# Kernel tuning notes

Measured on AMD Instinct MI355X. Metric: run time of the kernel, lower is better.

The kernel has to match this reference:

```python
import jax, jax.numpy as jnp
import numpy as np

HIDDEN = 2048
N_HEADS = 32
N_KV_HEADS = 8
HEAD_DIM = HIDDEN // N_HEADS  # 64
N_REP = N_HEADS // N_KV_HEADS  # 4
ROPE_THETA = 10000.0


def setup_inputs() -> dict:
    key = jax.random.key(0)
    ks = jax.random.split(key, 5)
    b, s = 2, 2048
    x = jax.random.normal(ks[0], (b, s, HIDDEN), dtype=jnp.float32)
    position_ids = jnp.arange(b * s, dtype=jnp.int32).reshape(b, s)
    sc = 1.0 / np.sqrt(HIDDEN)
    Wq = jax.random.normal(ks[1], (HIDDEN, HIDDEN), dtype=jnp.float32) * sc
    Wk = jax.random.normal(ks[2], (HIDDEN, N_KV_HEADS * HEAD_DIM), dtype=jnp.float32) * sc
    Wv = jax.random.normal(ks[3], (HIDDEN, N_KV_HEADS * HEAD_DIM), dtype=jnp.float32) * sc
    Wo = jax.random.normal(ks[4], (HIDDEN, HIDDEN), dtype=jnp.float32) * sc
    return {"input_ids": x, "Wq": Wq, "Wk": Wk, "Wv": Wv, "Wo": Wo,
            "position_ids": position_ids}


def _rope_cos_sin(position_ids, dtype):
    # inv_freq: [head_dim/2]
    inv_freq = 1.0 / (ROPE_THETA ** (jnp.arange(0, HEAD_DIM, 2, dtype=jnp.float32) / HEAD_DIM))
    freqs = position_ids.astype(jnp.float32)[..., None] * inv_freq  # [b, s, d/2]
    emb = jnp.concatenate([freqs, freqs], axis=-1)  # [b, s, d]
    return emb.astype(dtype), None  # placeholder, replaced below


def _rotate_half(x):
    x1, x2 = jnp.split(x, 2, axis=-1)
    return jnp.concatenate([-x2, x1], axis=-1)


def reference(input_ids, Wq, Wk, Wv, Wo, position_ids):
    b, s, _ = input_ids.shape
    q = (input_ids @ Wq).reshape(b, s, N_HEADS, HEAD_DIM).transpose(0, 2, 1, 3)      # [b,H,s,d]
    k = (input_ids @ Wk).reshape(b, s, N_KV_HEADS, HEAD_DIM).transpose(0, 2, 1, 3)   # [b,Hkv,s,d]
    v = (input_ids @ Wv).reshape(b, s, N_KV_HEADS, HEAD_DIM).transpose(0, 2, 1, 3)

    # RoPE
    inv_freq = 1.0 / (ROPE_THETA ** (jnp.arange(0, HEAD_DIM, 2, dtype=jnp.float32) / HEAD_DIM))
    freqs = position_ids.astype(jnp.float32)[..., None] * inv_freq  # [b,s,d/2]
    emb = jnp.concatenate([freqs, freqs], axis=-1)                   # [b,s,d]
    cos = jnp.cos(emb).astype(input_ids.dtype)[:, None, :, :]        # [b,1,s,d]
    sin = jnp.sin(emb).astype(input_ids.dtype)[:, None, :, :]
    q = q * cos + _rotate_half(q) * sin
    k = k * cos + _rotate_half(k) * sin

    # repeat_kv: [b,Hkv,s,d] -> [b,H,s,d]
    k = jnp.repeat(k, N_REP, axis=1)
    v = jnp.repeat(v, N_REP, axis=1)

    # causal SDPA
    scale = 1.0 / np.sqrt(HEAD_DIM)
    scores = jnp.einsum('bhqd,bhkd->bhqk', q, k) * scale
    causal = jnp.tril(jnp.ones((s, s), dtype=bool))
    scores = jnp.where(causal, scores, jnp.finfo(scores.dtype).min)
    attn = jax.nn.softmax(scores, axis=-1)
    out = jnp.einsum('bhqk,bhkd->bhqd', attn, v)                     # [b,H,s,d]
    out = out.transpose(0, 2, 1, 3).reshape(b, s, HIDDEN)
    return out @ Wo
```

## Files before the change

### kernel.cpp

```cpp
#include <hip/hip_runtime.h>
#include <hip/hip_bf16.h>

#define HIDDEN 2048
#define NHEADS 32
#define NKVH   8
#define HD     64
#define BATCH  2
#define SEQ    2048
#define ROWS   (BATCH * SEQ)
#define NQKV   3072
#define KCOL   2048
#define VCOL   2560

typedef __bf16 bf16x8 __attribute__((ext_vector_type(8)));
typedef __bf16 bf16x4 __attribute__((ext_vector_type(4)));
typedef float  f32x4  __attribute__((ext_vector_type(4)));
typedef short  s16x4  __attribute__((ext_vector_type(4)));
typedef short  s16x8  __attribute__((ext_vector_type(8)));

__device__ __forceinline__ void gl2lds16(const void* g, void* l) {
  __builtin_amdgcn_global_load_lds(
      (const __attribute__((address_space(1))) void*)g,
      (__attribute__((address_space(3))) void*)l, 16, 0, 0);
}

__device__ __forceinline__ short f2bs(float f) {
  __bf16 h = (__bf16)f;
  return __builtin_bit_cast(short, h);
}

__device__ __forceinline__ f32x4 mfma16(s16x4 a, s16x4 b, f32x4 c) {
#if __has_builtin(__builtin_amdgcn_mfma_f32_16x16x16bf16_1k)
  return __builtin_amdgcn_mfma_f32_16x16x16bf16_1k(a, b, c, 0, 0, 0);
#else
  s16x8 a8 = __builtin_shufflevector(a, (s16x4){0,0,0,0}, 0,1,2,3,4,5,6,7);
  s16x8 b8 = __builtin_shufflevector(b, (s16x4){0,0,0,0}, 0,1,2,3,4,5,6,7);
  a8[4]=0;a8[5]=0;a8[6]=0;a8[7]=0; b8[4]=0;b8[5]=0;b8[6]=0;b8[7]=0;
  return __builtin_amdgcn_mfma_f32_16x16x32_bf16(
      __builtin_bit_cast(bf16x8, a8), __builtin_bit_cast(bf16x8, b8), c, 0, 0, 0);
#endif
}

__global__ void prep(const float* __restrict__ Wq, const float* __restrict__ Wk,
                     const float* __restrict__ Wv, const float* __restrict__ Wo,
                     const float* __restrict__ x,
                     __bf16* __restrict__ dstW, __bf16* __restrict__ Xb) {
  __shared__ __bf16 tile[32][33];
  int bid = blockIdx.x, tid = threadIdx.x;
  if (bid < 10240) {
    int n0 = (bid % 160) * 32, k0 = (bid / 160) * 32;
    int tx = tid & 31, ty = tid >> 5;
    const float* src;
    int N, c0;
    if (n0 < 2048)      { src = Wq; N = 2048; c0 = n0; }
    else if (n0 < 2560) { src = Wk; N = 512;  c0 = n0 - 2048; }
    else if (n0 < 3072) { src = Wv; N = 512;  c0 = n0 - 2560; }
    else                { src = Wo; N = 2048; c0 = n0 - 3072; }
#pragma unroll
    for (int i = 0; i < 32; i += 8)
      tile[ty + i][tx] = (__bf16)src[(size_t)(k0 + ty + i) * N + (c0 + tx)];
    __syncthreads();
#pragma unroll
    for (int i = 0; i < 32; i += 8)
      dstW[(size_t)(n0 + ty + i) * HIDDEN + (k0 + tx)] = tile[tx][ty + i];
  } else {
    size_t i = (size_t)(bid - 10240) * 256 + tid;
    const float4* s = (const float4*)(x + i * 16);
    float4 a = s[0], b = s[1], c = s[2], d = s[3];
    bf16x8 o0, o1;
    o0[0] = (__bf16)a.x; o0[1] = (__bf16)a.y; o0[2] = (__bf16)a.z; o0[3] = (__bf16)a.w;
    o0[4] = (__bf16)b.x; o0[5] = (__bf16)b.y; o0[6] = (__bf16)b.z; o0[7] = (__bf16)b.w;
    o1[0] = (__bf16)c.x; o1[1] = (__bf16)c.y; o1[2] = (__bf16)c.z; o1[3] = (__bf16)c.w;
    o1[4] = (__bf16)d.x; o1[5] = (__bf16)d.y; o1[6] = (__bf16)d.z; o1[7] = (__bf16)d.w;
    *(bf16x8*)(Xb + i * 16)     = o0;
    *(bf16x8*)(Xb + i * 16 + 8) = o1;
  }
}

template <typename OutT, bool ROPE>
__launch_bounds__(256, 2)
__global__ void gemm_bt(const __bf16* __restrict__ A, const __bf16* __restrict__ Bt,
                        OutT* __restrict__ C, int M, int N, int K,
                        const int* __restrict__ pos_ids, __bf16* __restrict__ Vt) {
  __shared__ __bf16 As[2][128 * 32];
  __shared__ __bf16 Bs[2][128 * 32];
  int id = blockIdx.x;
  int bm = (id & 7) * 4 + ((id >> 3) & 3);
  int bn = id >> 5;
  int t = threadIdx.x;
  int wave = t >> 6, lane = t & 63, l16 = lane & 15, quad = lane >> 4;
  int wm = (wave >> 1) * 64, wn = (wave & 1) * 64;

  f32x4 acc[4][4] = {};

  int arow = t >> 2;
  int ac   = (t & 3) * 8;
  const __bf16* Ag = A  + (size_t)(bm * 128 + arow) * K + ac;
  const __bf16* Bg = Bt + (size_t)(bn * 128 + arow) * K + ac;
  int woff = wave * 512;

  for (int k0 = 0; k0 < K; k0 += 64) {
    __syncthreads();
    gl2lds16(Ag + k0,                      &As[0][woff]);
    gl2lds16(Ag + (size_t)64 * K + k0,      &As[0][2048 + woff]);
    gl2lds16(Ag + k0 + 32,                 &As[1][woff]);
    gl2lds16(Ag + (size_t)64 * K + k0 + 32, &As[1][2048 + woff]);
    gl2lds16(Bg + k0,                      &Bs[0][woff]);
    gl2lds16(Bg + (size_t)64 * K + k0,      &Bs[0][2048 + woff]);
    gl2lds16(Bg + k0 + 32,                 &Bs[1][woff]);
    gl2lds16(Bg + (size_t)64 * K + k0 + 32, &Bs[1][2048 + woff]);
    __syncthreads();

#pragma unroll
    for (int ks = 0; ks < 2; ++ks) {
      bf16x8 af[4], bfr[4];
#pragma unroll
      for (int i = 0; i < 4; ++i) {
        af[i]  = *(const bf16x8*)(&As[ks][(wm + i * 16 + l16) * 32 + quad * 8]);
        bfr[i] = *(const bf16x8*)(&Bs[ks][(wn + i * 16 + l16) * 32 + quad * 8]);
      }
#pragma unroll
      for (int i = 0; i < 4; ++i)
#pragma unroll
        for (int j = 0; j < 4; ++j)
          acc[i][j] = __builtin_amdgcn_mfma_f32_16x16x32_bf16(af[i], bfr[j], acc[i][j], 0, 0, 0);
    }
  }

  if (ROPE) {
    int headidx = bn * 2 + (wn >> 6);
    if (headidx >= 40) {
#pragma unroll
      for (int i = 0; i < 4; ++i) {
        int srow = bm * 128 + wm + i * 16 + quad * 4;
        int b = srow >> 11, s = srow & 2047;
#pragma unroll
        for (int j = 0; j < 4; ++j) {
          int vcol = bn * 128 + wn + j * 16 + l16 - VCOL;
          int hk = vcol >> 6, d = vcol & 63;
          bf16x4 w;
#pragma unroll
          for (int r = 0; r < 4; ++r) w[r] = (__bf16)acc[i][j][r];
          *(bf16x4*)(Vt + ((size_t)(b * NKVH + hk) * HD + d) * SEQ + s) = w;
        }
      }
      return;
    }
    float invrev0 = __expf(-(float)l16 * 0.28782313662425574f) * 0.15915494309189535f;
    float invrev1 = __expf(-(float)(l16 + 16) * 0.28782313662425574f) * 0.15915494309189535f;
#pragma unroll
    for (int i = 0; i < 4; ++i)
#pragma unroll
      for (int r = 0; r < 4; ++r) {
        int gr = bm * 128 + wm + i * 16 + quad * 4 + r;
        float pos = (float)pos_ids[gr];
        float rv0 = pos * invrev0; rv0 -= floorf(rv0);
        float rv1 = pos * invrev1; rv1 -= floorf(rv1);
        float a0 = rv0 * 6.283185307179586f, a1 = rv1 * 6.283185307179586f;
        float s0 = __sinf(a0), c0 = __cosf(a0);
        float s1 = __sinf(a1), c1 = __cosf(a1);
        float x0 = acc[i][0][r], x2 = acc[i][2][r];
        acc[i][0][r] = x0 * c0 - x2 * s0;
        acc[i][2][r] = x2 * c0 + x0 * s0;
        float x1 = acc[i][1][r], x3 = acc[i][3][r];
        acc[i][1][r] = x1 * c1 - x3 * s1;
        acc[i][3][r] = x3 * c1 + x1 * s1;
      }
  }

#pragma unroll
  for (int i = 0; i < 4; ++i)
#pragma unroll
    for (int j = 0; j < 4; ++j)
#pragma unroll
      for (int r = 0; r < 4; ++r)
        C[(size_t)(bm * 128 + wm + i * 16 + quad * 4 + r) * N +
          (bn * 128 + wn + j * 16 + l16)] = (OutT)acc[i][j][r];
}

__launch_bounds__(256, 3)
__global__ void flash_attn(const __bf16* __restrict__ QKV, const __bf16* __restrict__ Vt,
                           __bf16* __restrict__ O) {
  int p = blockIdx.x >> 1, h2 = blockIdx.x & 1;
  int hk = blockIdx.y, b = blockIdx.z;
  int t = threadIdx.x;
  int wave = t >> 6, lane = t & 63, l16 = lane & 15, quad = lane >> 4;
  int hh = h2 * 2 + (wave >> 1);
  int h  = hk * 4 + hh;
  int qs = wave & 1;

  __shared__ __bf16 Ks[2][2][64 * 32];
  __shared__ __bf16 Vs[2][4096];

  const __bf16* Kbase = QKV + (size_t)(b * SEQ) * NQKV + KCOL + hk * HD;
  const __bf16* VtB   = Vt + (size_t)(b * NKVH + hk) * HD * SEQ;

  int kr = wave * 16 + (lane >> 2);
  int kc = (lane & 3) * 8;
  int vd = wave * 16 + (lane >> 2);
  int vsc = (lane & 3) * 16;
  int vs4w = (lane & 3) * 4;

  for (int seg = 0; seg < 2; ++seg) {
    int qt = seg ? (31 - p) : p;

    __syncthreads();

    bf16x8 qfrag[2][2];
#pragma unroll
    for (int qi = 0; qi < 2; ++qi) {
      const __bf16* qp = QKV + (size_t)(b * SEQ + qt * 64 + qs * 32 + qi * 16 + l16) * NQKV
                       + h * HD + quad * 8;
      bf16x8 q0 = *(const bf16x8*)qp;
      bf16x8 q1 = *(const bf16x8*)(qp + 32);
#pragma unroll
      for (int e = 0; e < 8; ++e) {
        qfrag[qi][0][e] = (__bf16)((float)q0[e] * 0.125f);
        qfrag[qi][1][e] = (__bf16)((float)q1[e] * 0.125f);
      }
    }

    float lsum[2] = {0.f, 0.f};
    f32x4 oacc[2][4];
#pragma unroll
    for (int qi = 0; qi < 2; ++qi)
#pragma unroll
      for (int dt = 0; dt < 4; ++dt) oacc[qi][dt] = (f32x4){0.f, 0.f, 0.f, 0.f};

    {
      const __bf16* kp = Kbase + (size_t)kr * NQKV + kc;
      gl2lds16(kp,      &Ks[0][0][wave * 512]);
      gl2lds16(kp + 32, &Ks[0][1][wave * 512]);
      const __bf16* vp = VtB + (size_t)vd * SEQ + vsc;
      s16x8 v0 = __builtin_bit_cast(s16x8, *(const bf16x8*)vp);
      s16x8 v1 = __builtin_bit_cast(s16x8, *(const bf16x8*)(vp + 8));
      *(s16x4*)(&Vs[0][(vs4w + 0) * 256 + vd * 4]) = __builtin_shufflevector(v0, v0, 0, 1, 2, 3);
      *(s16x4*)(&Vs[0][(vs4w + 1) * 256 + vd * 4]) = __builtin_shufflevector(v0, v0, 4, 5, 6, 7);
      *(s16x4*)(&Vs[0][(vs4w + 2) * 256 + vd * 4]) = __builtin_shufflevector(v1, v1, 0, 1, 2, 3);
      *(s16x4*)(&Vs[0][(vs4w + 3) * 256 + vd * 4]) = __builtin_shufflevector(v1, v1, 4, 5, 6, 7);
    }

    for (int kt = 0; kt <= qt; ++kt) {
      int buf = kt & 1;
      __syncthreads();

      bool pre = (kt < qt);
      s16x8 pv0, pv1;
      if (pre) {
        const __bf16* kp = Kbase + (size_t)((kt + 1) * 64 + kr) * NQKV + kc;
        gl2lds16(kp,      &Ks[buf ^ 1][0][wave * 512]);
        gl2lds16(kp + 32, &Ks[buf ^ 1][1][wave * 512]);
        const __bf16* vp = VtB + (size_t)vd * SEQ + (kt + 1) * 64 + vsc;
        pv0 = __builtin_bit_cast(s16x8, *(const bf16x8*)vp);
        pv1 = __builtin_bit_cast(s16x8, *(const bf16x8*)(vp + 8));
      }

      f32x4 sacc[2][4];
#pragma unroll
      for (int qi = 0; qi < 2; ++qi)
#pragma unroll
        for (int nt = 0; nt < 4; ++nt) sacc[qi][nt] = (f32x4){0.f, 0.f, 0.f, 0.f};
#pragma unroll
      for (int ks = 0; ks < 2; ++ks) {
        bf16x8 kf[4];
#pragma unroll
        for (int nt = 0; nt < 4; ++nt)
          kf[nt] = *(const bf16x8*)(&Ks[buf][ks][(nt * 16 + l16) * 32 + quad * 8]);
#pragma unroll
        for (int nt = 0; nt < 4; ++nt)
#pragma unroll
          for (int qi = 0; qi < 2; ++qi)
            sacc[qi][nt] = __builtin_amdgcn_mfma_f32_16x16x32_bf16(kf[nt], qfrag[qi][ks], sacc[qi][nt], 0, 0, 0);
      }

      s16x4 af[2][4];
      if (kt == qt) {
#pragma unroll
        for (int qi = 0; qi < 2; ++qi)
#pragma unroll
          for (int nt = 0; nt < 4; ++nt)
#pragma unroll
            for (int r = 0; r < 4; ++r) {
              int kg = nt * 16 + quad * 4 + r;
              int qg = qs * 32 + qi * 16 + l16;
              float e = __expf((kg > qg) ? -1e30f : sacc[qi][nt][r]);
              lsum[qi] += e;
              af[qi][nt][r] = f2bs(e);
            }
      } else {
#pragma unroll
        for (int qi = 0; qi < 2; ++qi)
#pragma unroll
          for (int nt = 0; nt < 4; ++nt)
#pragma unroll
            for (int r = 0; r < 4; ++r) {
              float e = __expf(sacc[qi][nt][r]);
              lsum[qi] += e;
              af[qi][nt][r] = f2bs(e);
            }
      }

#pragma unroll
      for (int nt = 0; nt < 4; ++nt) {
        s16x4 vf[4];
#pragma unroll
        for (int dt = 0; dt < 4; ++dt)
          vf[dt] = *(const s16x4*)(&Vs[buf][(nt * 4 + quad) * 256 + (dt * 16 + l16) * 4]);
#pragma unroll
        for (int qi = 0; qi < 2; ++qi)
#pragma unroll
          for (int dt = 0; dt < 4; ++dt)
            oacc[qi][dt] = mfma16(af[qi][nt], vf[dt], oacc[qi][dt]);
      }

      if (pre) {
        *(s16x4*)(&Vs[buf ^ 1][(vs4w + 0) * 256 + vd * 4]) = __builtin_shufflevector(pv0, pv0, 0, 1, 2, 3);
        *(s16x4*)(&Vs[buf ^ 1][(vs4w + 1) * 256 + vd * 4]) = __builtin_shufflevector(pv0, pv0, 4, 5, 6, 7);
        *(s16x4*)(&Vs[buf ^ 1][(vs4w + 2) * 256 + vd * 4]) = __builtin_shufflevector(pv1, pv1, 0, 1, 2, 3);
        *(s16x4*)(&Vs[buf ^ 1][(vs4w + 3) * 256 + vd * 4]) = __builtin_shufflevector(pv1, pv1, 4, 5, 6, 7);
      }
    }

#pragma unroll
    for (int qi = 0; qi < 2; ++qi) {
      float l = lsum[qi];
      l += __shfl_xor(l, 16);
      l += __shfl_xor(l, 32);
#pragma unroll
      for (int r = 0; r < 4; ++r) {
        float lr = __shfl(l, quad * 4 + r);
        float inv = 1.0f / lr;
#pragma unroll
        for (int dt = 0; dt < 4; ++dt) {
          float o = oacc[qi][dt][r] * inv;
          O[(size_t)(b * SEQ + qt * 64 + qs * 32 + qi * 16 + quad * 4 + r) * HIDDEN +
            h * HD + dt * 16 + l16] = (__bf16)o;
        }
      }
    }
  }
}

extern "C" void kernel_launch(void* const* d_in, const int* in_sizes, int n_in,
                              void* d_out, int out_size, void* d_ws, size_t ws_size,
                              hipStream_t stream) {
  const float* x  = (const float*)d_in[0];
  const float* Wq = (const float*)d_in[1];
  const float* Wk = (const float*)d_in[2];
  const float* Wv = (const float*)d_in[3];
  const float* Wo = (const float*)d_in[4];
  const int* pos  = (const int*)d_in[5];

  __bf16* Wqkvt = (__bf16*)d_ws;
  __bf16* Wot   = Wqkvt + (size_t)NQKV * HIDDEN;
  __bf16* Xb    = Wot + (size_t)HIDDEN * HIDDEN;
  __bf16* QKV   = Xb + (size_t)ROWS * HIDDEN;
  __bf16* Oat   = QKV + (size_t)ROWS * NQKV;
  __bf16* Vt    = Xb;

  prep<<<dim3(12288), 256, 0, stream>>>(Wq, Wk, Wv, Wo, x, Wqkvt, Xb);

  gemm_bt<__bf16, true><<<dim3(768), 256, 0, stream>>>(
      Xb, Wqkvt, QKV, ROWS, NQKV, HIDDEN, pos, Vt);

  flash_attn<<<dim3(32, NKVH, BATCH), 256, 0, stream>>>(QKV, Vt, Oat);

  gemm_bt<float, false><<<dim3(512), 256, 0, stream>>>(
      Oat, Wot, (float*)d_out, ROWS, HIDDEN, HIDDEN, nullptr, nullptr);
}
```

Baseline: 280.6 us.

## Repartition flash attention to one head per block with MFMA row sums and exp2

Each attention workgroup now handles a single query head, with each wave owning 16 query rows, and the grid doubles to 1024 blocks under an XCD-aware swizzle. Softmax uses exp2 with the log2(e) factor folded into the Q scale, and the row sums are accumulated by an extra MFMA against a ones vector instead of scalar adds and shuffles. Register use drops, allowing 4 blocks per CU. The cost is that each K/V tile is now loaded by four blocks per KV head instead of two, which raises L2 and global traffic.

```diff
diff --git a/kernel.cpp b/kernel.cpp
--- a/kernel.cpp
+++ b/kernel.cpp
@@ -27,6 +27,14 @@
 __device__ __forceinline__ short f2bs(float f) {
   __bf16 h = (__bf16)f;
   return __builtin_bit_cast(short, h);
+}
+
+__device__ __forceinline__ float fexp2(float x) {
+#if __has_builtin(__builtin_amdgcn_exp2f)
+  return __builtin_amdgcn_exp2f(x);
+#else
+  return exp2f(x);
+#endif
 }
 
 __device__ __forceinline__ f32x4 mfma16(s16x4 a, s16x4 b, f32x4 c) {
@@ -178,16 +186,19 @@
           (bn * 128 + wn + j * 16 + l16)] = (OutT)acc[i][j][r];
 }
 
-__launch_bounds__(256, 3)
+__launch_bounds__(256, 4)
 __global__ void flash_attn(const __bf16* __restrict__ QKV, const __bf16* __restrict__ Vt,
                            __bf16* __restrict__ O) {
-  int p = blockIdx.x >> 1, h2 = blockIdx.x & 1;
-  int hk = blockIdx.y, b = blockIdx.z;
+  int wgid = blockIdx.x + 64 * (blockIdx.y + 8 * (int)blockIdx.z);
+  int swz  = (wgid & 7) * 128 + (wgid >> 3);
+  int b  = swz >> 9;
+  int hk = (swz >> 6) & 7;
+  int bx = swz & 63;
+  int p  = bx >> 2;
+  int h  = hk * 4 + (bx & 3);
+
   int t = threadIdx.x;
   int wave = t >> 6, lane = t & 63, l16 = lane & 15, quad = lane >> 4;
-  int hh = h2 * 2 + (wave >> 1);
-  int h  = hk * 4 + hh;
-  int qs = wave & 1;
 
   __shared__ __bf16 Ks[2][2][64 * 32];
   __shared__ __bf16 Vs[2][4096];
@@ -201,31 +212,30 @@
   int vsc = (lane & 3) * 16;
   int vs4w = (lane & 3) * 4;
 
+  const s16x4 vones = { (short)0x3F80, (short)0x3F80, (short)0x3F80, (short)0x3F80 };
+
   for (int seg = 0; seg < 2; ++seg) {
     int qt = seg ? (31 - p) : p;
 
     __syncthreads();
 
-    bf16x8 qfrag[2][2];
-#pragma unroll
-    for (int qi = 0; qi < 2; ++qi) {
-      const __bf16* qp = QKV + (size_t)(b * SEQ + qt * 64 + qs * 32 + qi * 16 + l16) * NQKV
+    bf16x8 qfrag[2];
+    {
+      const __bf16* qp = QKV + (size_t)(b * SEQ + qt * 64 + wave * 16 + l16) * NQKV
                        + h * HD + quad * 8;
       bf16x8 q0 = *(const bf16x8*)qp;
       bf16x8 q1 = *(const bf16x8*)(qp + 32);
 #pragma unroll
       for (int e = 0; e < 8; ++e) {
-        qfrag[qi][0][e] = (__bf16)((float)q0[e] * 0.125f);
-        qfrag[qi][1][e] = (__bf16)((float)q1[e] * 0.125f);
-      }
-    }
-
-    float lsum[2] = {0.f, 0.f};
-    f32x4 oacc[2][4];
-#pragma unroll
-    for (int qi = 0; qi < 2; ++qi)
-#pragma unroll
-      for (int dt = 0; dt < 4; ++dt) oacc[qi][dt] = (f32x4){0.f, 0.f, 0.f, 0.f};
+        qfrag[0][e] = (__bf16)((float)q0[e] * 0.18033688011112042f);
+        qfrag[1][e] = (__bf16)((float)q1[e] * 0.18033688011112042f);
+      }
+    }
+
+    f32x4 lacc = {0.f, 0.f, 0.f, 0.f};
+    f32x4 oacc[4];
+#pragma unroll
+    for (int dt = 0; dt < 4; ++dt) oacc[dt] = (f32x4){0.f, 0.f, 0.f, 0.f};
 
     {
       const __bf16* kp = Kbase + (size_t)kr * NQKV + kc;
@@ -255,11 +265,9 @@
         pv1 = __builtin_bit_cast(s16x8, *(const bf16x8*)(vp + 8));
       }
 
-      f32x4 sacc[2][4];
-#pragma unroll
-      for (int qi = 0; qi < 2; ++qi)
-#pragma unroll
-        for (int nt = 0; nt < 4; ++nt) sacc[qi][nt] = (f32x4){0.f, 0.f, 0.f, 0.f};
+      f32x4 sacc[4];
+#pragma unroll
+      for (int nt = 0; nt < 4; ++nt) sacc[nt] = (f32x4){0.f, 0.f, 0.f, 0.f};
 #pragma unroll
       for (int ks = 0; ks < 2; ++ks) {
         bf16x8 kf[4];
@@ -268,36 +276,26 @@
           kf[nt] = *(const bf16x8*)(&Ks[buf][ks][(nt * 16 + l16) * 32 + quad * 8]);
 #pragma unroll
         for (int nt = 0; nt < 4; ++nt)
-#pragma unroll
-          for (int qi = 0; qi < 2; ++qi)
-            sacc[qi][nt] = __builtin_amdgcn_mfma_f32_16x16x32_bf16(kf[nt], qfrag[qi][ks], sacc[qi][nt], 0, 0, 0);
-      }
-
-      s16x4 af[2][4];
+          sacc[nt] = __builtin_amdgcn_mfma_f32_16x16x32_bf16(kf[nt], qfrag[ks], sacc[nt], 0, 0, 0);
+      }
+
+      s16x4 af[4];
       if (kt == qt) {
-#pragma unroll
-        for (int qi = 0; qi < 2; ++qi)
-#pragma unroll
-          for (int nt = 0; nt < 4; ++nt)
-#pragma unroll
-            for (int r = 0; r < 4; ++r) {
-              int kg = nt * 16 + quad * 4 + r;
-              int qg = qs * 32 + qi * 16 + l16;
-              float e = __expf((kg > qg) ? -1e30f : sacc[qi][nt][r]);
-              lsum[qi] += e;
-              af[qi][nt][r] = f2bs(e);
-            }
+        int qg = wave * 16 + l16;
+#pragma unroll
+        for (int nt = 0; nt < 4; ++nt)
+#pragma unroll
+          for (int r = 0; r < 4; ++r) {
+            int kg = nt * 16 + quad * 4 + r;
+            float e = fexp2((kg > qg) ? -1e30f : sacc[nt][r]);
+            af[nt][r] = f2bs(e);
+          }
       } else {
 #pragma unroll
-        for (int qi = 0; qi < 2; ++qi)
-#pragma unroll
-          for (int nt = 0; nt < 4; ++nt)
-#pragma unroll
-            for (int r = 0; r < 4; ++r) {
-              float e = __expf(sacc[qi][nt][r]);
-              lsum[qi] += e;
-              af[qi][nt][r] = f2bs(e);
-            }
+        for (int nt = 0; nt < 4; ++nt)
+#pragma unroll
+          for (int r = 0; r < 4; ++r)
+            af[nt][r] = f2bs(fexp2(sacc[nt][r]));
       }
 
 #pragma unroll
@@ -307,10 +305,9 @@
         for (int dt = 0; dt < 4; ++dt)
           vf[dt] = *(const s16x4*)(&Vs[buf][(nt * 4 + quad) * 256 + (dt * 16 + l16) * 4]);
 #pragma unroll
-        for (int qi = 0; qi < 2; ++qi)
-#pragma unroll
-          for (int dt = 0; dt < 4; ++dt)
-            oacc[qi][dt] = mfma16(af[qi][nt], vf[dt], oacc[qi][dt]);
+        for (int dt = 0; dt < 4; ++dt)
+          oacc[dt] = mfma16(af[nt], vf[dt], oacc[dt]);
+        lacc = mfma16(af[nt], vones, lacc);
       }
 
       if (pre) {
@@ -322,20 +319,13 @@
     }
 
 #pragma unroll
-    for (int qi = 0; qi < 2; ++qi) {
-      float l = lsum[qi];
-      l += __shfl_xor(l, 16);
-      l += __shfl_xor(l, 32);
-#pragma unroll
-      for (int r = 0; r < 4; ++r) {
-        float lr = __shfl(l, quad * 4 + r);
-        float inv = 1.0f / lr;
-#pragma unroll
-        for (int dt = 0; dt < 4; ++dt) {
-          float o = oacc[qi][dt][r] * inv;
-          O[(size_t)(b * SEQ + qt * 64 + qs * 32 + qi * 16 + quad * 4 + r) * HIDDEN +
-            h * HD + dt * 16 + l16] = (__bf16)o;
-        }
+    for (int r = 0; r < 4; ++r) {
+      float inv = 1.0f / lacc[r];
+#pragma unroll
+      for (int dt = 0; dt < 4; ++dt) {
+        float o = oacc[dt][r] * inv;
+        O[(size_t)(b * SEQ + qt * 64 + wave * 16 + quad * 4 + r) * HIDDEN +
+          h * HD + dt * 16 + l16] = (__bf16)o;
       }
     }
   }
@@ -363,7 +353,7 @@
   gemm_bt<__bf16, true><<<dim3(768), 256, 0, stream>>>(
       Xb, Wqkvt, QKV, ROWS, NQKV, HIDDEN, pos, Vt);
 
-  flash_attn<<<dim3(32, NKVH, BATCH), 256, 0, stream>>>(QKV, Vt, Oat);
+  flash_attn<<<dim3(64, NKVH, BATCH), 256, 0, stream>>>(QKV, Vt, Oat);
 
   gemm_bt<float, false><<<dim3(512), 256, 0, stream>>>(
       Oat, Wot, (float*)d_out, ROWS, HIDDEN, HIDDEN, nullptr, nullptr);
```

Result: no change. 276.8 us (-1.4%).
